# Performance work log

Measured on AMD Instinct MI355X. Metric: run time of the kernel, lower is better.

Reference implementation:

```python
import jax, jax.numpy as jnp
import numpy as np
from jax import lax

N_LAYER = 4
D_MODEL = 1024
D_INNER = 2048   # expand=2
D_STATE = 16
DT_RANK = 64     # ceil(d_model/16)
D_CONV = 4
BATCH = 2
SEQ = 2048
EPS = 1e-5


def setup_inputs() -> dict:
    key = jax.random.key(0)
    ks = jax.random.split(key, 8)
    rn = lambda k, shape, s=0.02: jax.random.normal(k, shape, dtype=jnp.float32) * s
    # S4D-real init for A_log, as in mamba_ssm
    A_init = jnp.tile(jnp.arange(1, D_STATE + 1, dtype=jnp.float32)[None, None, :],
                      (N_LAYER, D_INNER, 1))
    return {
        "hidden_states": jax.random.normal(ks[0], (BATCH, SEQ, D_MODEL), dtype=jnp.float32),
        "norm_w": jnp.ones((N_LAYER, D_MODEL), jnp.float32),
        "norm_b": jnp.zeros((N_LAYER, D_MODEL), jnp.float32),
        "in_proj_w": rn(ks[1], (N_LAYER, 2 * D_INNER, D_MODEL)),
        "conv_w": rn(ks[2], (N_LAYER, D_INNER, D_CONV), 0.1),
        "conv_b": jnp.zeros((N_LAYER, D_INNER), jnp.float32),
        "x_proj_w": rn(ks[3], (N_LAYER, DT_RANK + 2 * D_STATE, D_INNER)),
        "dt_proj_w": rn(ks[4], (N_LAYER, D_INNER, DT_RANK), 0.1),
        "dt_proj_b": rn(ks[5], (N_LAYER, D_INNER), 0.1),
        "A_log": jnp.log(A_init),
        "D": jnp.ones((N_LAYER, D_INNER), jnp.float32),
        "out_proj_w": rn(ks[6], (N_LAYER, D_MODEL, D_INNER)),
        "final_norm_w": jnp.ones((D_MODEL,), jnp.float32),
        "final_norm_b": jnp.zeros((D_MODEL,), jnp.float32),
    }


def _layernorm(x, w, b):
    mu = jnp.mean(x, axis=-1, keepdims=True)
    var = jnp.mean(jnp.square(x - mu), axis=-1, keepdims=True)
    return (x - mu) * lax.rsqrt(var + EPS) * w + b


def _mamba_block(h, in_w, conv_w, conv_b, x_w, dt_w, dt_b, A_log, Dp, out_w):
    B, L, _ = h.shape
    xz = jnp.einsum('bld,ed->ble', h, in_w)               # [B,L,2*d_inner]
    x, z = jnp.split(xz, 2, axis=-1)
    # depthwise causal conv1d (kernel D_CONV), truncated to L
    xp = jnp.pad(x, ((0, 0), (D_CONV - 1, 0), (0, 0)))
    x = sum(xp[:, k:k + L, :] * conv_w[:, k] for k in range(D_CONV)) + conv_b
    x = jax.nn.silu(x)
    x_dbl = jnp.einsum('bld,ed->ble', x, x_w)             # [B,L,dt_rank+2*d_state]
    dt, Bm, Cm = jnp.split(x_dbl, [DT_RANK, DT_RANK + D_STATE], axis=-1)
    delta = jax.nn.softplus(jnp.einsum('blr,dr->bld', dt, dt_w) + dt_b)  # [B,L,d_inner]
    A = -jnp.exp(A_log)                                   # [d_inner, d_state]

    def step(state, xs):
        d_t, B_t, C_t, u_t = xs                           # [B,di],[B,ds],[B,ds],[B,di]
        dA = jnp.exp(d_t[..., None] * A)                  # [B,di,ds]
        state = dA * state + (d_t * u_t)[..., None] * B_t[:, None, :]
        y_t = jnp.einsum('bds,bs->bd', state, C_t)
        return state, y_t

    xs = (jnp.swapaxes(delta, 0, 1), jnp.swapaxes(Bm, 0, 1),
          jnp.swapaxes(Cm, 0, 1), jnp.swapaxes(x, 0, 1))
    init = jnp.zeros((B, D_INNER, D_STATE), dtype=h.dtype)
    _, ys = lax.scan(step, init, xs)                      # ys: [L,B,di]
    y = jnp.swapaxes(ys, 0, 1) + x * Dp
    y = y * jax.nn.silu(z)
    return jnp.einsum('bld,ed->ble', y, out_w)            # [B,L,d_model]


def reference(hidden_states, norm_w, norm_b, in_proj_w, conv_w, conv_b,
              x_proj_w, dt_proj_w, dt_proj_b, A_log, D, out_proj_w,
              final_norm_w, final_norm_b):
    residual = None
    for i in range(N_LAYER):
        residual = hidden_states + residual if residual is not None else hidden_states
        h = _layernorm(residual, norm_w[i], norm_b[i])
        hidden_states = _mamba_block(h, in_proj_w[i], conv_w[i], conv_b[i],
                                     x_proj_w[i], dt_proj_w[i], dt_proj_b[i],
                                     A_log[i], D[i], out_proj_w[i])
    residual = hidden_states + residual
    return _layernorm(residual, final_norm_w, final_norm_b)
```

## Files before the change

### kernel.cpp

```cpp
#include <hip/hip_runtime.h>
#include <math.h>

#define N_LAYERS 4
#define DMODEL 1024
#define DINNER 2048
#define DSTATE 16
#define DTRANK 64
#define DCONV 4
#define NBATCH 2
#define LSEQ 2048
#define LNEPS 1e-5f
#define ROWS (NBATCH * LSEQ)
#define CLEN 32
#define NCHUNK (LSEQ / CLEN)
#define XP 128
#define KSLICE 256
#define NSLICE (DINNER / KSLICE)
#define OPSLICE 2

typedef __attribute__((ext_vector_type(8))) short bf16x8;
typedef __attribute__((ext_vector_type(8))) unsigned short ushort8;
typedef __attribute__((ext_vector_type(4))) float f32x4;
typedef __attribute__((ext_vector_type(4))) unsigned int uint4v;

__device__ __forceinline__ unsigned short f2bf(float f) {
  unsigned int u = __float_as_uint(f);
  return (unsigned short)((u + 0x7FFFu + ((u >> 16) & 1u)) >> 16);
}
__device__ __forceinline__ float bf2f(unsigned short h) {
  return __uint_as_float(((unsigned int)h) << 16);
}

__device__ __forceinline__ void gload16(const unsigned short* g, unsigned short* l) {
  __builtin_amdgcn_global_load_lds(
      (const __attribute__((address_space(1))) unsigned int*)g,
      (__attribute__((address_space(3))) unsigned int*)l, 16, 0, 0);
}

__device__ __forceinline__ float softplus_f(float x) {
  float e = __expf(-fabsf(x));
  return fmaxf(x, 0.f) + __logf(1.f + e);
}

__global__ __launch_bounds__(256) void cvt_f2bf(const float* __restrict__ src,
                                                unsigned short* __restrict__ dst, int n4) {
  int i = blockIdx.x * 256 + threadIdx.x;
  if (i >= n4) return;
  float4 v = ((const float4*)src)[i];
  ushort4 o;
  o.x = f2bf(v.x); o.y = f2bf(v.y); o.z = f2bf(v.z); o.w = f2bf(v.w);
  ((ushort4*)dst)[i] = o;
}

__global__ __launch_bounds__(256) void cvt_xpw(const float* __restrict__ src,
                                               unsigned short* __restrict__ dst) {
  int i = blockIdx.x * 256 + threadIdx.x;
  int col4 = i & 511;
  int row = (i >> 9) & 127;
  int layer = i >> 16;
  float4 v = make_float4(0.f, 0.f, 0.f, 0.f);
  if (row < 96) v = ((const float4*)(src + ((size_t)layer * 96 + row) * 2048))[col4];
  ushort4 o;
  o.x = f2bf(v.x); o.y = f2bf(v.y); o.z = f2bf(v.z); o.w = f2bf(v.w);
  ((ushort4*)(dst + ((size_t)layer * 128 + row) * 2048))[col4] = o;
}

template<bool OBF>
__global__ __launch_bounds__(256) void ln_kernel(
    const float* __restrict__ src, float* __restrict__ res_copy,
    const float* __restrict__ w, const float* __restrict__ b, void* out) {
  int row = blockIdx.x;
  int t = threadIdx.x;
  const float4* srow = (const float4*)(src + (size_t)row * DMODEL);
  float4 v = srow[t];
  if (res_copy) ((float4*)(res_copy + (size_t)row * DMODEL))[t] = v;
  float s = v.x + v.y + v.z + v.w;
  float sq = v.x * v.x + v.y * v.y + v.z * v.z + v.w * v.w;
  #pragma unroll
  for (int o = 32; o >= 1; o >>= 1) {
    s += __shfl_xor(s, o);
    sq += __shfl_xor(sq, o);
  }
  __shared__ float ss[4], ssq[4];
  int wid = t >> 6, lane = t & 63;
  if (lane == 0) { ss[wid] = s; ssq[wid] = sq; }
  __syncthreads();
  s = ss[0] + ss[1] + ss[2] + ss[3];
  sq = ssq[0] + ssq[1] + ssq[2] + ssq[3];
  float mu = s * (1.f / DMODEL);
  float var = sq * (1.f / DMODEL) - mu * mu;
  float rs = rsqrtf(var + LNEPS);
  float4 wv = ((const float4*)w)[t];
  float4 bv = ((const float4*)b)[t];
  float4 o4;
  o4.x = (v.x - mu) * rs * wv.x + bv.x;
  o4.y = (v.y - mu) * rs * wv.y + bv.y;
  o4.z = (v.z - mu) * rs * wv.z + bv.z;
  o4.w = (v.w - mu) * rs * wv.w + bv.w;
  if (OBF) {
    ushort4 ob;
    ob.x = f2bf(o4.x); ob.y = f2bf(o4.y); ob.z = f2bf(o4.z); ob.w = f2bf(o4.w);
    ((ushort4*)((unsigned short*)out + (size_t)row * DMODEL))[t] = ob;
  } else {
    ((float4*)((float*)out + (size_t)row * DMODEL))[t] = o4;
  }
}

template<int ACT, bool BIAS, bool ADD, bool WF32, bool WBF>
__global__ __launch_bounds__(512) void gemm256(
    const unsigned short* __restrict__ A, int lda,
    const unsigned short* __restrict__ W, int ldw,
    float* __restrict__ C, int ldc, int K,
    const float* __restrict__ bias,
    const float* __restrict__ addsrc,
    unsigned short* __restrict__ Cb) {
  __shared__ unsigned short lds[2][2][256][64];
  const int t = threadIdx.x;
  const int lane = t & 63;
  const int wave = t >> 6;
  const int wr = wave >> 2;
  const int wc = wave & 3;
  const int m0 = blockIdx.y * 256, n0 = blockIdx.x * 256;

  const int srow = t >> 3;
  const int sslot = t & 7;
  const int frow = lane & 15;
  const int hi = lane >> 4;

  f32x4 acc[8][4];
  #pragma unroll
  for (int m = 0; m < 8; m++)
    #pragma unroll
    for (int n = 0; n < 4; n++) acc[m][n] = (f32x4){0.f, 0.f, 0.f, 0.f};

  const int NT = K / 64;

  auto stage = [&](int buf, int kt) {
    const int scol = (sslot << 3) + kt * 64;
    #pragma unroll
    for (int r = 0; r < 4; ++r) {
      int row = srow + (r << 6);
      gload16(A + (size_t)(m0 + row) * lda + scol, &lds[buf][0][row][sslot << 3]);
    }
    #pragma unroll
    for (int r = 0; r < 4; ++r) {
      int row = srow + (r << 6);
      gload16(W + (size_t)(n0 + row) * ldw + scol, &lds[buf][1][row][sslot << 3]);
    }
  };

  auto compute = [&](int buf) {
    #pragma unroll
    for (int ks = 0; ks < 2; ++ks) {
      bf16x8 a[8], b[4];
      #pragma unroll
      for (int m = 0; m < 8; ++m) {
        int row = wr * 128 + m * 16 + frow;
        a[m] = *(const bf16x8*)&lds[buf][0][row][(ks * 4 + hi) << 3];
      }
      #pragma unroll
      for (int n = 0; n < 4; ++n) {
        int row = wc * 64 + n * 16 + frow;
        b[n] = *(const bf16x8*)&lds[buf][1][row][(ks * 4 + hi) << 3];
      }
      __builtin_amdgcn_s_setprio(1);
      #pragma unroll
      for (int m = 0; m < 8; ++m)
        #pragma unroll
        for (int n = 0; n < 4; ++n)
          acc[m][n] = __builtin_amdgcn_mfma_f32_16x16x32_bf16(a[m], b[n], acc[m][n], 0, 0, 0);
      __builtin_amdgcn_s_setprio(0);
    }
  };

  stage(0, 0);
  if (NT > 1) stage(1, 1);
  for (int kt = 0; kt < NT - 1; ++kt) {
    asm volatile("s_waitcnt vmcnt(8)" ::: "memory");
    __builtin_amdgcn_s_barrier();
    asm volatile("" ::: "memory");
    compute(kt & 1);
    __builtin_amdgcn_s_barrier();
    asm volatile("" ::: "memory");
    if (kt + 2 < NT) stage(kt & 1, kt + 2);
  }
  asm volatile("s_waitcnt vmcnt(0)" ::: "memory");
  __builtin_amdgcn_s_barrier();
  asm volatile("" ::: "memory");
  compute((NT - 1) & 1);

  #pragma unroll
  for (int m = 0; m < 8; ++m) {
    int rbase = m0 + wr * 128 + m * 16 + hi * 4;
    #pragma unroll
    for (int n = 0; n < 4; ++n) {
      int ccol = n0 + wc * 64 + n * 16 + frow;
      #pragma unroll
      for (int j = 0; j < 4; ++j) {
        int crow = rbase + j;
        float v = acc[m][n][j];
        if (BIAS) v += bias[ccol];
        if (ACT == 1) v = softplus_f(v);
        if (ADD) v += addsrc[(size_t)crow * ldc + ccol];
        if (WF32) C[(size_t)crow * ldc + ccol] = v;
        if (WBF) Cb[(size_t)crow * ldc + ccol] = f2bf(v);
      }
    }
  }
}

template<int ACT, bool BIAS, bool ADD, bool WF32, bool WBF, bool PARTIAL>
__global__ __launch_bounds__(256) void gemm_bf16(
    const unsigned short* __restrict__ A, int lda,
    const unsigned short* __restrict__ W, int ldw,
    float* __restrict__ C, int ldc, int K,
    const float* __restrict__ bias,
    const float* __restrict__ addsrc,
    unsigned short* __restrict__ Cb) {
  __shared__ unsigned short As[2][128][32];
  __shared__ unsigned short Ws[2][128][32];
  int t = threadIdx.x;
  int lane = t & 63, wave = t >> 6;
  int wr = wave >> 1, wc = wave & 1;
  int m0 = blockIdx.y * 128, n0 = blockIdx.x * 128;

  int kbase = 0;
  if (PARTIAL) {
    kbase = blockIdx.z * K;
    C += (size_t)blockIdx.z * (size_t)gridDim.y * 128 * ldc;
  }

  int r0 = t >> 2;
  int kk8 = (t & 3) << 3;
  const unsigned short* Ag = A + (size_t)(m0 + r0) * lda + kbase + kk8;
  const unsigned short* Wg = W + (size_t)(n0 + r0) * ldw + kbase + kk8;
  const size_t Astep = (size_t)64 * lda;
  const size_t Wstep = (size_t)64 * ldw;

  f32x4 zero = {0.f, 0.f, 0.f, 0.f};
  f32x4 acc[4][4];
  #pragma unroll
  for (int m = 0; m < 4; m++)
    #pragma unroll
    for (int n = 0; n < 4; n++) acc[m][n] = zero;

  int frow = lane & 15;
  int fk = (lane >> 4) << 3;

  auto stage = [&](int buf, int kt) {
    const unsigned short* ag = Ag + kt * 32;
    const unsigned short* wg = Wg + kt * 32;
    unsigned short* la = &As[buf][r0][kk8];
    unsigned short* lw = &Ws[buf][r0][kk8];
    gload16(ag, la);
    gload16(ag + Astep, la + 64 * 32);
    gload16(wg, lw);
    gload16(wg + Wstep, lw + 64 * 32);
  };
  auto compute = [&](int buf) {
    bf16x8 af[4], bw[4];
    #pragma unroll
    for (int m = 0; m < 4; m++)
      af[m] = *(const bf16x8*)&As[buf][wr * 64 + m * 16 + frow][fk];
    #pragma unroll
    for (int n = 0; n < 4; n++)
      bw[n] = *(const bf16x8*)&Ws[buf][wc * 64 + n * 16 + frow][fk];
    #pragma unroll
    for (int m = 0; m < 4; m++)
      #pragma unroll
      for (int n = 0; n < 4; n++)
        acc[m][n] = __builtin_amdgcn_mfma_f32_16x16x32_bf16(af[m], bw[n], acc[m][n], 0, 0, 0);
  };

  const int NT = K / 32;
  stage(0, 0);
  __syncthreads();
  int cur = 0;
  for (int kt = 0; kt < NT - 1; ++kt) {
    stage(cur ^ 1, kt + 1);
    compute(cur);
    __syncthreads();
    cur ^= 1;
  }
  compute(cur);

  #pragma unroll
  for (int m = 0; m < 4; m++) {
    int rbase = m0 + wr * 64 + m * 16 + ((lane >> 4) << 2);
    #pragma unroll
    for (int n = 0; n < 4; n++) {
      int ccol = n0 + wc * 64 + n * 16 + (lane & 15);
      #pragma unroll
      for (int j = 0; j < 4; j++) {
        int crow = rbase + j;
        float v = acc[m][n][j];
        if (BIAS) v += bias[ccol];
        if (ACT == 1) v = softplus_f(v);
        if (ADD) v += addsrc[(size_t)crow * ldc + ccol];
        if (WF32 || PARTIAL) C[(size_t)crow * ldc + ccol] = v;
        if (WBF) Cb[(size_t)crow * ldc + ccol] = f2bf(v);
      }
    }
  }
}

__global__ __launch_bounds__(256) void combine_xdbl(
    const float* __restrict__ part, float* __restrict__ xdbl,
    unsigned short* __restrict__ xdbl_bf) {
  int i = blockIdx.x * 256 + threadIdx.x;
  const size_t slab = (size_t)ROWS * XP / 4;
  const float4* p = (const float4*)part;
  float4 s = make_float4(0.f, 0.f, 0.f, 0.f);
  #pragma unroll
  for (int z = 0; z < NSLICE; z++) {
    float4 a = p[i + (size_t)z * slab];
    s.x += a.x; s.y += a.y; s.z += a.z; s.w += a.w;
  }
  ((float4*)xdbl)[i] = s;
  ushort4 o;
  o.x = f2bf(s.x); o.y = f2bf(s.y); o.z = f2bf(s.z); o.w = f2bf(s.w);
  ((ushort4*)xdbl_bf)[i] = o;
}

__global__ __launch_bounds__(256) void combine_residual(
    const float* __restrict__ part, float* __restrict__ residual) {
  int i = blockIdx.x * 256 + threadIdx.x;
  const size_t slab = (size_t)ROWS * DMODEL / 4;
  const float4* p = (const float4*)part;
  float4 a = p[i], b = p[i + slab];
  float4 r = ((const float4*)residual)[i];
  r.x += a.x + b.x;
  r.y += a.y + b.y;
  r.z += a.z + b.z;
  r.w += a.w + b.w;
  ((float4*)residual)[i] = r;
}

__global__ __launch_bounds__(256) void conv_silu_kernel(
    const unsigned short* __restrict__ xz, const float* __restrict__ cw,
    const float* __restrict__ cb, unsigned short* __restrict__ xbf) {
  int tid = blockIdx.x * 256 + threadIdx.x;
  int dv = tid & (DINNER / 8 - 1);
  int rg = tid >> 8;
  int l0 = (rg & (LSEQ / 4 - 1)) * 4;
  int row0 = rg * 4;
  int d = dv * 8;

  float4 wq[8];
  #pragma unroll
  for (int j = 0; j < 8; j++) wq[j] = ((const float4*)(cw + (size_t)d * DCONV))[j];
  float4 b0 = ((const float4*)(cb + d))[0];
  float4 b1 = ((const float4*)(cb + d))[1];
  const float bias[8] = {b0.x, b0.y, b0.z, b0.w, b1.x, b1.y, b1.z, b1.w};

  ushort8 xin[7];
  #pragma unroll
  for (int r = 0; r < 7; r++) {
    int l = l0 - 3 + r;
    if (l >= 0)
      xin[r] = *(const ushort8*)(xz + (size_t)(row0 - 3 + r) * (2 * DINNER) + d);
    else
      xin[r] = (ushort8){0, 0, 0, 0, 0, 0, 0, 0};
  }

  #pragma unroll
  for (int o = 0; o < 4; o++) {
    ushort8 ob;
    #pragma unroll
    for (int j = 0; j < 8; j++) {
      const float* wj = (const float*)&wq[j];
      float acc = bias[j];
      #pragma unroll
      for (int k = 0; k < DCONV; k++)
        acc = fmaf(bf2f(xin[o + k][j]), wj[k], acc);
      float s = acc / (1.f + __expf(-acc));
      ob[j] = f2bf(s);
    }
    *(ushort8*)(xbf + (size_t)(row0 + o) * DINNER + d) = ob;
  }
}

__global__ __launch_bounds__(256) void scan_p1(
    const float* __restrict__ delta, const unsigned short* __restrict__ u,
    const float* __restrict__ xdbl, const float* __restrict__ A_log,
    unsigned int* __restrict__ carrybuf) {
  int tid = blockIdx.x * 256 + threadIdx.x;
  int t = threadIdx.x;
  int d = tid & (DINNER - 1);
  int chunk = (tid >> 11) & (NCHUNK - 1);
  int b = tid >> 17;
  int l0 = chunk * CLEN;

  __shared__ float bl[CLEN][16];
  {
    const float4* src4 = (const float4*)(xdbl + ((size_t)b * LSEQ + l0) * XP);
    if (t < CLEN * 4) {
      int li = t >> 2, qi = t & 3;
      ((float4*)&bl[li][0])[qi] = src4[li * (XP / 4) + 16 + qi];
    }
  }
  __syncthreads();

  float A[DSTATE], st[DSTATE], ap[DSTATE];
  const float4* Ar = (const float4*)(A_log + d * DSTATE);
  #pragma unroll
  for (int q = 0; q < 4; q++) {
    float4 av = Ar[q];
    A[4 * q] = -__expf(av.x); A[4 * q + 1] = -__expf(av.y);
    A[4 * q + 2] = -__expf(av.z); A[4 * q + 3] = -__expf(av.w);
  }
  #pragma unroll
  for (int s = 0; s < DSTATE; s++) { st[s] = 0.f; ap[s] = 1.f; }

  const float* dptr = delta + ((size_t)b * LSEQ + l0) * DINNER + d;
  const unsigned short* uptr = u + ((size_t)b * LSEQ + l0) * DINNER + d;
  float dt_n = dptr[0];
  float uu_n = bf2f(uptr[0]);
  #pragma unroll 4
  for (int l = 0; l < CLEN; l++) {
    float dt = dt_n, uu = uu_n;
    if (l + 1 < CLEN) {
      dt_n = dptr[(size_t)(l + 1) * DINNER];
      uu_n = bf2f(uptr[(size_t)(l + 1) * DINNER]);
    }
    float du = dt * uu;
    #pragma unroll
    for (int q = 0; q < 4; q++) {
      float4 B4 = *(const float4*)&bl[l][q * 4];
      const float Bj[4] = {B4.x, B4.y, B4.z, B4.w};
      #pragma unroll
      for (int j = 0; j < 4; j++) {
        int s = 4 * q + j;
        float dA = __expf(dt * A[s]);
        st[s] = fmaf(dA, st[s], du * Bj[j]);
        ap[s] *= dA;
      }
    }
  }
  uint4v* co = (uint4v*)(carrybuf + (size_t)tid * DSTATE);
  #pragma unroll
  for (int q = 0; q < 4; q++) {
    uint4v v;
    #pragma unroll
    for (int j = 0; j < 4; j++)
      v[j] = ((unsigned int)f2bf(ap[4 * q + j]) << 16) | f2bf(st[4 * q + j]);
    co[q] = v;
  }
}

__global__ __launch_bounds__(256) void scan_p2(
    const unsigned int* __restrict__ cbuf, unsigned short* __restrict__ carryin) {
  int tid = blockIdx.x * 256 + threadIdx.x;
  int ds = tid & (DINNER * DSTATE - 1);
  int b = tid >> 15;
  float carry = 0.f;
  size_t base = (size_t)b * NCHUNK * DINNER * DSTATE + ds;
  const size_t cs = DINNER * DSTATE;
  for (int c = 0; c < NCHUNK; c += 4) {
    size_t i0 = base + (size_t)c * cs;
    unsigned int v0 = cbuf[i0], v1 = cbuf[i0 + cs];
    unsigned int v2 = cbuf[i0 + 2 * cs], v3 = cbuf[i0 + 3 * cs];
    carryin[i0] = f2bf(carry);
    carry = fmaf(bf2f(v0 >> 16), carry, bf2f(v0 & 0xFFFFu));
    carryin[i0 + cs] = f2bf(carry);
    carry = fmaf(bf2f(v1 >> 16), carry, bf2f(v1 & 0xFFFFu));
    carryin[i0 + 2 * cs] = f2bf(carry);
    carry = fmaf(bf2f(v2 >> 16), carry, bf2f(v2 & 0xFFFFu));
    carryin[i0 + 3 * cs] = f2bf(carry);
    carry = fmaf(bf2f(v3 >> 16), carry, bf2f(v3 & 0xFFFFu));
  }
}

__global__ __launch_bounds__(256) void scan_p3(
    const float* __restrict__ delta, const unsigned short* __restrict__ u,
    const float* __restrict__ xdbl, const unsigned short* __restrict__ xzbf,
    const float* __restrict__ A_log, const float* __restrict__ Dp,
    const unsigned short* __restrict__ carryin, unsigned short* __restrict__ ybf) {
  int tid = blockIdx.x * 256 + threadIdx.x;
  int t = threadIdx.x;
  int d = tid & (DINNER - 1);
  int chunk = (tid >> 11) & (NCHUNK - 1);
  int b = tid >> 17;
  int l0 = chunk * CLEN;

  __shared__ float bc[CLEN][32];
  {
    const float4* src4 = (const float4*)(xdbl + ((size_t)b * LSEQ + l0) * XP);
    int li = t >> 3, qi = t & 7;
    ((float4*)&bc[li][0])[qi] = src4[li * (XP / 4) + 16 + qi];
  }
  __syncthreads();

  float A[DSTATE], st[DSTATE];
  {
    const ushort8* ci8 = (const ushort8*)(carryin + (size_t)tid * DSTATE);
    ushort8 c0 = ci8[0], c1 = ci8[1];
    #pragma unroll
    for (int j = 0; j < 8; j++) { st[j] = bf2f(c0[j]); st[8 + j] = bf2f(c1[j]); }
  }
  const float4* Ar = (const float4*)(A_log + d * DSTATE);
  #pragma unroll
  for (int q = 0; q < 4; q++) {
    float4 av = Ar[q];
    A[4 * q] = -__expf(av.x); A[4 * q + 1] = -__expf(av.y);
    A[4 * q + 2] = -__expf(av.z); A[4 * q + 3] = -__expf(av.w);
  }
  float Dval = Dp[d];

  const float* dptr = delta + ((size_t)b * LSEQ + l0) * DINNER + d;
  const unsigned short* uptr = u + ((size_t)b * LSEQ + l0) * DINNER + d;
  const unsigned short* zptr = xzbf + ((size_t)b * LSEQ + l0) * (2 * DINNER) + DINNER + d;
  unsigned short* yptr = ybf + ((size_t)b * LSEQ + l0) * DINNER + d;

  float dt_n = dptr[0];
  float uu_n = bf2f(uptr[0]);
  float zz_n = bf2f(zptr[0]);
  #pragma unroll 4
  for (int l = 0; l < CLEN; l++) {
    float dt = dt_n, uu = uu_n, zz = zz_n;
    if (l + 1 < CLEN) {
      dt_n = dptr[(size_t)(l + 1) * DINNER];
      uu_n = bf2f(uptr[(size_t)(l + 1) * DINNER]);
      zz_n = bf2f(zptr[(size_t)(l + 1) * (2 * DINNER)]);
    }
    float du = dt * uu;
    #pragma unroll
    for (int q = 0; q < 4; q++) {
      float4 B4 = *(const float4*)&bc[l][q * 4];
      const float Bj[4] = {B4.x, B4.y, B4.z, B4.w};
      #pragma unroll
      for (int j = 0; j < 4; j++) {
        int s = 4 * q + j;
        float dA = __expf(dt * A[s]);
        st[s] = fmaf(dA, st[s], du * Bj[j]);
      }
    }
    float acc = 0.f;
    #pragma unroll
    for (int q = 0; q < 4; q++) {
      float4 C4 = *(const float4*)&bc[l][16 + q * 4];
      const float Cj[4] = {C4.x, C4.y, C4.z, C4.w};
      #pragma unroll
      for (int j = 0; j < 4; j++) acc = fmaf(st[4 * q + j], Cj[j], acc);
    }
    float yv = (acc + uu * Dval) * (zz / (1.f + __expf(-zz)));
    yptr[(size_t)l * DINNER] = f2bf(yv);
  }
}

extern "C" void kernel_launch(void* const* d_in, const int* in_sizes, int n_in,
                              void* d_out, int out_size, void* d_ws, size_t ws_size,
                              hipStream_t stream) {
  const float* hidden    = (const float*)d_in[0];
  const float* norm_w    = (const float*)d_in[1];
  const float* norm_b    = (const float*)d_in[2];
  const float* in_proj_w = (const float*)d_in[3];
  const float* conv_w    = (const float*)d_in[4];
  const float* conv_b    = (const float*)d_in[5];
  const float* x_proj_w  = (const float*)d_in[6];
  const float* dt_proj_w = (const float*)d_in[7];
  const float* dt_proj_b = (const float*)d_in[8];
  const float* A_log     = (const float*)d_in[9];
  const float* Dp        = (const float*)d_in[10];
  const float* out_proj_w= (const float*)d_in[11];
  const float* fnw       = (const float*)d_in[12];
  const float* fnb       = (const float*)d_in[13];
  float* out = (float*)d_out;

  const size_t CARRYSZ = (size_t)NBATCH * NCHUNK * DINNER * DSTATE;

  float* residual = (float*)d_ws;
  float* delta    = residual + (size_t)ROWS * DMODEL;
  float* xdbl     = delta + (size_t)ROWS * DINNER;
  float* fend     = xdbl + (size_t)ROWS * XP;

  unsigned short* xz_bf   = (unsigned short*)fend;
  unsigned short* xbuf_bf = xz_bf + (size_t)ROWS * 2 * DINNER;
  unsigned short* h_bf    = xbuf_bf + (size_t)ROWS * DINNER;
  unsigned short* ybuf_bf = h_bf + (size_t)ROWS * DMODEL;
  unsigned short* xdbl_bf = ybuf_bf + (size_t)ROWS * DINNER;
  unsigned short* xpw_bf  = xdbl_bf + (size_t)ROWS * XP;
  unsigned short* dtw_bf  = xpw_bf + (size_t)N_LAYERS * XP * DINNER;
  unsigned short* ipw_bf  = dtw_bf + (size_t)N_LAYERS * DINNER * DTRANK;
  unsigned short* opw_bf  = ipw_bf + (size_t)2 * DINNER * DMODEL;
  unsigned short* usend   = opw_bf + (size_t)DMODEL * DINNER;

  unsigned int*   carrybuf = (unsigned int*)usend;
  unsigned short* carryin  = (unsigned short*)(carrybuf + CARRYSZ);
  float*          xpart    = delta;
  float*          oppart   = delta;

  cvt_xpw<<<N_LAYERS * XP * DINNER / 4 / 256, 256, 0, stream>>>(x_proj_w, xpw_bf);
  {
    int n4 = N_LAYERS * DINNER * DTRANK / 4;
    cvt_f2bf<<<n4 / 256, 256, 0, stream>>>(dt_proj_w, dtw_bf, n4);
  }

  for (int i = 0; i < N_LAYERS; i++) {
    {
      int n4 = 2 * DINNER * DMODEL / 4;
      cvt_f2bf<<<n4 / 256, 256, 0, stream>>>(
          in_proj_w + (size_t)i * 2 * DINNER * DMODEL, ipw_bf, n4);
      n4 = DMODEL * DINNER / 4;
      cvt_f2bf<<<n4 / 256, 256, 0, stream>>>(
          out_proj_w + (size_t)i * DMODEL * DINNER, opw_bf, n4);
    }
    ln_kernel<true><<<ROWS, 256, 0, stream>>>(
        i == 0 ? hidden : residual, i == 0 ? residual : nullptr,
        norm_w + (size_t)i * DMODEL, norm_b + (size_t)i * DMODEL, h_bf);
    {
      dim3 g(2 * DINNER / 256, ROWS / 256);
      gemm256<0, false, false, false, true><<<g, 512, 0, stream>>>(
          h_bf, DMODEL, ipw_bf, DMODEL, nullptr, 2 * DINNER, DMODEL,
          nullptr, nullptr, xz_bf);
    }
    conv_silu_kernel<<<ROWS / 4 * DINNER / 8 / 256, 256, 0, stream>>>(
        xz_bf, conv_w + (size_t)i * DINNER * DCONV, conv_b + (size_t)i * DINNER,
        xbuf_bf);
    {
      dim3 g(1, ROWS / 128, NSLICE);
      gemm_bf16<0, false, false, true, false, true><<<g, 256, 0, stream>>>(
          xbuf_bf, DINNER, xpw_bf + (size_t)i * XP * DINNER, DINNER,
          xpart, XP, KSLICE, nullptr, nullptr, nullptr);
      combine_xdbl<<<ROWS * XP / 4 / 256, 256, 0, stream>>>(xpart, xdbl, xdbl_bf);
    }
    {
      dim3 g(DINNER / 128, ROWS / 128);
      gemm_bf16<1, true, false, true, false, false><<<g, 256, 0, stream>>>(
          xdbl_bf, XP, dtw_bf + (size_t)i * DINNER * DTRANK, DTRANK,
          delta, DINNER, DTRANK, dt_proj_b + (size_t)i * DINNER,
          nullptr, nullptr);
    }
    scan_p1<<<NBATCH * NCHUNK * DINNER / 256, 256, 0, stream>>>(
        delta, xbuf_bf, xdbl, A_log + (size_t)i * DINNER * DSTATE, carrybuf);
    scan_p2<<<NBATCH * DINNER * DSTATE / 256, 256, 0, stream>>>(carrybuf, carryin);
    scan_p3<<<NBATCH * NCHUNK * DINNER / 256, 256, 0, stream>>>(
        delta, xbuf_bf, xdbl, xz_bf, A_log + (size_t)i * DINNER * DSTATE,
        Dp + (size_t)i * DINNER, carryin, ybuf_bf);
    {
      dim3 g(DMODEL / 128, ROWS / 128, OPSLICE);
      gemm_bf16<0, false, false, false, false, true><<<g, 256, 0, stream>>>(
          ybuf_bf, DINNER, opw_bf, DINNER,
          oppart, DMODEL, DINNER / OPSLICE, nullptr, nullptr, nullptr);
      combine_residual<<<ROWS * DMODEL / 4 / 256, 256, 0, stream>>>(oppart, residual);
    }
  }
  ln_kernel<false><<<ROWS, 256, 0, stream>>>(residual, nullptr, fnw, fnb, out);
}
```

Measured before the change: 897.4 us.

## Stage in_proj GEMM tiles through registers into padded single-buffer LDS

The 256x256 in_proj GEMM no longer uses direct global-to-LDS async loads with a double buffer. Each tile is prefetched into registers while the current tile is computed, then written to a single LDS buffer whose rows are padded to 72 elements to reduce bank conflicts on fragment reads. This halves LDS use and avoids conflicted reads, but adds an extra barrier per iteration, more register pressure from the staging registers, and exposes the LDS write latency.

```diff
diff --git a/kernel.cpp b/kernel.cpp
--- a/kernel.cpp
+++ b/kernel.cpp
@@ -107,26 +107,26 @@
 }
 
 template<int ACT, bool BIAS, bool ADD, bool WF32, bool WBF>
-__global__ __launch_bounds__(512) void gemm256(
+__global__ __launch_bounds__(512) void gemm256r(
     const unsigned short* __restrict__ A, int lda,
     const unsigned short* __restrict__ W, int ldw,
     float* __restrict__ C, int ldc, int K,
     const float* __restrict__ bias,
     const float* __restrict__ addsrc,
     unsigned short* __restrict__ Cb) {
-  __shared__ unsigned short lds[2][2][256][64];
+  __shared__ unsigned short lds[2][256][72];
   const int t = threadIdx.x;
   const int lane = t & 63;
   const int wave = t >> 6;
   const int wr = wave >> 2;
   const int wc = wave & 3;
   const int m0 = blockIdx.y * 256, n0 = blockIdx.x * 256;
-
-  const int srow = t >> 3;
-  const int sslot = t & 7;
   const int frow = lane & 15;
   const int hi = lane >> 4;
 
+  const int srow = t >> 3;
+  const int sc8 = (t & 7) << 3;
+
   f32x4 acc[8][4];
   #pragma unroll
   for (int m = 0; m < 8; m++)
@@ -134,35 +134,34 @@
     for (int n = 0; n < 4; n++) acc[m][n] = (f32x4){0.f, 0.f, 0.f, 0.f};
 
   const int NT = K / 64;
-
-  auto stage = [&](int buf, int kt) {
-    const int scol = (sslot << 3) + kt * 64;
+  ushort8 areg[4], wreg[4];
+
+  auto loadreg = [&](int kt) {
     #pragma unroll
     for (int r = 0; r < 4; ++r) {
       int row = srow + (r << 6);
-      gload16(A + (size_t)(m0 + row) * lda + scol, &lds[buf][0][row][sslot << 3]);
-    }
+      areg[r] = *(const ushort8*)(A + (size_t)(m0 + row) * lda + kt * 64 + sc8);
+      wreg[r] = *(const ushort8*)(W + (size_t)(n0 + row) * ldw + kt * 64 + sc8);
+    }
+  };
+  auto dswrite = [&]() {
     #pragma unroll
     for (int r = 0; r < 4; ++r) {
       int row = srow + (r << 6);
-      gload16(W + (size_t)(n0 + row) * ldw + scol, &lds[buf][1][row][sslot << 3]);
+      *(ushort8*)&lds[0][row][sc8] = areg[r];
+      *(ushort8*)&lds[1][row][sc8] = wreg[r];
     }
   };
-
-  auto compute = [&](int buf) {
+  auto compute = [&]() {
     #pragma unroll
     for (int ks = 0; ks < 2; ++ks) {
       bf16x8 a[8], b[4];
       #pragma unroll
-      for (int m = 0; m < 8; ++m) {
-        int row = wr * 128 + m * 16 + frow;
-        a[m] = *(const bf16x8*)&lds[buf][0][row][(ks * 4 + hi) << 3];
-      }
-      #pragma unroll
-      for (int n = 0; n < 4; ++n) {
-        int row = wc * 64 + n * 16 + frow;
-        b[n] = *(const bf16x8*)&lds[buf][1][row][(ks * 4 + hi) << 3];
-      }
+      for (int m = 0; m < 8; ++m)
+        a[m] = *(const bf16x8*)&lds[0][wr * 128 + m * 16 + frow][(ks * 4 + hi) << 3];
+      #pragma unroll
+      for (int n = 0; n < 4; ++n)
+        b[n] = *(const bf16x8*)&lds[1][wc * 64 + n * 16 + frow][(ks * 4 + hi) << 3];
       __builtin_amdgcn_s_setprio(1);
       #pragma unroll
       for (int m = 0; m < 8; ++m)
@@ -173,21 +172,18 @@
     }
   };
 
-  stage(0, 0);
-  if (NT > 1) stage(1, 1);
-  for (int kt = 0; kt < NT - 1; ++kt) {
-    asm volatile("s_waitcnt vmcnt(8)" ::: "memory");
-    __builtin_amdgcn_s_barrier();
-    asm volatile("" ::: "memory");
-    compute(kt & 1);
-    __builtin_amdgcn_s_barrier();
-    asm volatile("" ::: "memory");
-    if (kt + 2 < NT) stage(kt & 1, kt + 2);
-  }
-  asm volatile("s_waitcnt vmcnt(0)" ::: "memory");
-  __builtin_amdgcn_s_barrier();
-  asm volatile("" ::: "memory");
-  compute((NT - 1) & 1);
+  loadreg(0);
+  dswrite();
+  __syncthreads();
+  for (int kt = 0; kt < NT; ++kt) {
+    if (kt + 1 < NT) loadreg(kt + 1);
+    compute();
+    __syncthreads();
+    if (kt + 1 < NT) {
+      dswrite();
+      __syncthreads();
+    }
+  }
 
   #pragma unroll
   for (int m = 0; m < 8; ++m) {
@@ -610,7 +606,7 @@
         norm_w + (size_t)i * DMODEL, norm_b + (size_t)i * DMODEL, h_bf);
     {
       dim3 g(2 * DINNER / 256, ROWS / 256);
-      gemm256<0, false, false, false, true><<<g, 512, 0, stream>>>(
+      gemm256r<0, false, false, false, true><<<g, 512, 0, stream>>>(
           h_bf, DMODEL, ipw_bf, DMODEL, nullptr, 2 * DINNER, DMODEL,
           nullptr, nullptr, xz_bf);
     }
```

Result: no change. 884.5 us (-1.4%).
